# Kernel tuning notes

Hardware: AMD Instinct MI355X
Metric: run time of the kernel (lower is better)

Reference implementation:

```python
import jax, jax.numpy as jnp
import numpy as np

N_VERT, D = 100000, 128
N_EDGE, K, R = 20000, 8, 4


def setup_inputs() -> dict:
    key = jax.random.key(0)
    ks = jax.random.split(key, 16)
    s = 0.05
    return {
        'feats': jax.random.normal(ks[0], (N_VERT, D), dtype=jnp.float32),
        'edge_members': jax.random.randint(ks[1], (N_EDGE, K), 0, N_VERT),
        'adj_members': jax.random.randint(ks[2], (N_EDGE, R, K), 0, N_VERT),
        'ids': jnp.arange(N_EDGE),
        'epoch': 10,
        # VertexConv params (Linear(d,1) each)
        'wq': jax.random.normal(ks[3], (D, 1)) * s, 'bq': jnp.zeros((1,)),
        'wk': jax.random.normal(ks[4], (D, 1)) * s, 'bk': jnp.zeros((1,)),
        'wv': jax.random.normal(ks[5], (D, 1)) * s, 'bv': jnp.zeros((1,)),
        # EdgeConv MLP: Linear(d, d//4) -> ReLU -> Linear(d//4, 1)
        'W1': jax.random.normal(ks[6], (D, D // 4)) * s, 'b1': jnp.zeros((D // 4,)),
        'W2': jax.random.normal(ks[7], (D // 4, 1)) * s, 'b2': jnp.zeros((1,)),
        # final classifier Linear(d, 2)
        'Wfc': jax.random.normal(ks[8], (D, 2)) * s, 'bfc': jnp.zeros((2,)),
    }


def _vertex_conv(feats, members, wq, bq, wk, bk, wv, bv):
    # members: [E, K] vertex indices; aggregates each hyperedge's vertices into one feature.
    f = feats[members]                         # [E,K,d] irregular gather
    q = f @ wq + bq                            # [E,K,1]
    k = f @ wk + bk                            # [E,K,1]
    v = f @ wv + bv                            # [E,K,1]
    # score[e,j,l] = q[e,j]*k[e,l]; original softmaxes over the K-1 "other" vertices (l != j)
    S = q * jnp.swapaxes(k, -1, -2)            # [E,K,K]
    S = jnp.where(jnp.eye(members.shape[-1], dtype=bool), -jnp.inf, S)
    a = jax.nn.softmax(S, axis=-1)             # [E,K,K]
    di = jnp.tanh(jnp.einsum('ejl,elo->ejo', a, v))  # [E,K,1] per-vertex scalar gate
    return (di * f).sum(axis=1)                # [E,d]


def reference(feats, edge_members, adj_members, ids, epoch,
              wq, bq, wk, bk, wv, bv, W1, b1, W2, b2, Wfc, bfc):
    n = edge_members.shape[0]
    # epoch >= wu_e(=0): hyperedge feature from edge_dict
    xn = _vertex_conv(feats, edge_members, wq, bq, wk, bk, wv, bv)   # [N,d]
    # epoch >= wu_a(=5): hyperedge features from each vertex's adjacent edges
    xe = _vertex_conv(feats, adj_members.reshape(n * R, K),
                      wq, bq, wk, bk, wv, bv).reshape(n, R, -1)       # [N,R,d]
    ft = jnp.concatenate([xn[:, None, :], xe], axis=1)                # [N,1+R,d]
    # EdgeConv: attention over the 1+R candidate hyperedge feats
    sc = jax.nn.relu(ft @ W1 + b1) @ W2 + b2                          # [N,1+R,1]
    a = jax.nn.softmax(sc, axis=1)
    h = (a * ft).sum(axis=1)                                          # [N,d]
    # dropout in eval mode (identity), then sigmoid(Linear(d,2))
    return jax.nn.sigmoid(h @ Wfc + bfc)                              # [N,2]
```

## Files before the change

kernel.cpp:

```cpp
#include <hip/hip_runtime.h>
#include <math.h>

#define KK 8
#define DD 128
#define RR 4
#define NG 5
#define HID 32
#define NSLOT 48

typedef __attribute__((ext_vector_type(8))) short short8_t;
typedef __attribute__((ext_vector_type(4))) float f32x4_t;

__device__ __forceinline__ unsigned short f2bf(float x) {
    unsigned int u = __float_as_uint(x);
    unsigned int r = (u + 0x7FFFu + ((u >> 16) & 1u)) >> 16;
    return (unsigned short)r;
}
__device__ __forceinline__ float bf2f(unsigned short u) {
    return __uint_as_float((unsigned int)u << 16);
}
__device__ __forceinline__ float fexp(float x) { return __expf(x); }
__device__ __forceinline__ float frcp(float x) { return __builtin_amdgcn_rcpf(x); }
__device__ __forceinline__ float ftanh(float x) {
    const float xx = fminf(fmaxf(x, -10.f), 10.f);
    const float e2 = __expf(2.f * xx);
    return (e2 - 1.f) * __builtin_amdgcn_rcpf(e2 + 1.f);
}

__global__ __launch_bounds__(256) void proj_mfma(
    const float* __restrict__ feats, int n_vert, int n_tg,
    const float* __restrict__ wq, const float* __restrict__ wk,
    const float* __restrict__ wv, const float* __restrict__ Wfc,
    const float* __restrict__ W1,
    const float* __restrict__ bq, const float* __restrict__ bk,
    const float* __restrict__ bv,
    unsigned short* __restrict__ proj)
{
    __shared__ short Bsh[12 * 64 * 8];

    const int t = threadIdx.x;
    const int wave = t >> 6, lane = t & 63;
    const int row = lane & 15;
    const int kg  = lane >> 4;

    #pragma unroll
    for (int q = 0; q < 3; ++q) {
        const int p = t + q * 256;
        const int ntks = p >> 6, plane = p & 63;
        const int nt = ntks >> 2, ks = ntks & 3;
        const int n  = nt * 16 + (plane & 15);
        const int k0 = ks * 32 + (plane >> 4) * 8;
        short8_t v;
        #pragma unroll
        for (int j = 0; j < 8; ++j) {
            const int k = k0 + j;
            float val;
            if      (n == 0) val = wq[k];
            else if (n == 1) val = wk[k];
            else if (n == 2) val = wv[k];
            else if (n == 3) val = Wfc[2 * k];
            else if (n == 4) val = Wfc[2 * k + 1];
            else if (n < 37) val = W1[k * HID + (n - 5)];
            else             val = 0.f;
            v[j] = (short)f2bf(val);
        }
        *(short8_t*)&Bsh[p * 8] = v;
    }

    const float bq0 = bq[0], bk0 = bk[0], bv0 = bv[0];
    __syncthreads();

    for (int tg = blockIdx.x; tg < n_tg; tg += gridDim.x) {
        const int mbase = (tg * 4 + wave) * 16;
        if (mbase >= n_vert) continue;

        long long arow = (long long)(mbase + row);
        if (arow >= n_vert) arow = n_vert - 1;
        const float* ar = &feats[arow * DD + kg * 8];
        float4 araw[8];
        #pragma unroll
        for (int ks = 0; ks < 4; ++ks) {
            araw[2 * ks]     = *(const float4*)&ar[ks * 32];
            araw[2 * ks + 1] = *(const float4*)&ar[ks * 32 + 4];
        }

        short8_t afrag[4];
        #pragma unroll
        for (int ks = 0; ks < 4; ++ks) {
            const float4 x0 = araw[2 * ks], x1 = araw[2 * ks + 1];
            short8_t a;
            a[0] = (short)f2bf(x0.x); a[1] = (short)f2bf(x0.y);
            a[2] = (short)f2bf(x0.z); a[3] = (short)f2bf(x0.w);
            a[4] = (short)f2bf(x1.x); a[5] = (short)f2bf(x1.y);
            a[6] = (short)f2bf(x1.z); a[7] = (short)f2bf(x1.w);
            afrag[ks] = a;
        }

        #pragma unroll
        for (int nt = 0; nt < 3; ++nt) {
            f32x4_t acc = {0.f, 0.f, 0.f, 0.f};
            #pragma unroll
            for (int ks = 0; ks < 4; ++ks) {
                const short8_t b = *(const short8_t*)&Bsh[((nt * 4 + ks) * 64 + lane) * 8];
                acc = __builtin_amdgcn_mfma_f32_16x16x32_bf16(afrag[ks], b, acc, 0, 0, 0);
            }
            const int col = nt * 16 + row;
            if (col < 37) {
                const int slot = (col < 5) ? col : (col + 3);
                float badd = 0.f;
                if      (col == 0) badd = bq0;
                else if (col == 1) badd = bk0;
                else if (col == 2) badd = bv0;
                #pragma unroll
                for (int r = 0; r < 4; ++r) {
                    const int vr = mbase + kg * 4 + r;
                    if (vr < n_vert)
                        proj[(long long)vr * NSLOT + slot] = f2bf(acc[r] + badd);
                }
            }
        }
    }
}

__global__ __launch_bounds__(256) void edge_fused(
    const int* __restrict__ edge_members,
    const int* __restrict__ adj_members,
    const unsigned short* __restrict__ proj,
    const float* __restrict__ b1, const float* __restrict__ W2,
    const float* __restrict__ b2, const float* __restrict__ bfc,
    float* __restrict__ out, int n_edge)
{
    __shared__ unsigned vidS[4][NG * KK];
    __shared__ float diS [4][NG * KK];
    __shared__ float ftfcS[4][NG][2];
    __shared__ float scS [4][NG];

    const int t = threadIdx.x;
    const int w = t >> 6;
    const int lane = t & 63;
    const int e = blockIdx.x * 4 + w;
    if (e >= n_edge) return;

    const int g = lane >> 3;
    const int j = lane & 7;
    const bool act = lane < NG * KK;

    int vid = 0;
    if (act) vid = (g == 0) ? edge_members[e * KK + j]
                            : adj_members[((e * RR) + (g - 1)) * KK + j];

    const char* projB = (const char*)proj;
    const unsigned vOff = (unsigned)vid * (NSLOT * 2u);

    const uint4 qpu = *(const uint4*)(projB + vOff);

    if (act) vidS[w][lane] = vOff;
    asm volatile("s_waitcnt lgkmcnt(0)" ::: "memory");

    const int m = lane & 31;
    const int h = lane >> 5;
    const unsigned mOff = 16u + 2u * (unsigned)m;
    float pv2[3][KK];
    #pragma unroll
    for (int p = 0; p < 3; ++p) {
        const int grp = (p << 1) | h;
        if (grp < NG) {
            #pragma unroll
            for (int r = 0; r < KK; ++r) {
                const unsigned off = vidS[w][grp * KK + r] + mOff;
                pv2[p][r] = bf2f(*(const unsigned short*)(projB + off));
            }
        }
    }

    const float qv  = bf2f((unsigned short)(qpu.x & 0xFFFFu));
    const float kv  = bf2f((unsigned short)(qpu.x >> 16));
    const float vv  = bf2f((unsigned short)(qpu.y & 0xFFFFu));
    const float pf0 = bf2f((unsigned short)(qpu.y >> 16));
    const float pf1 = bf2f((unsigned short)(qpu.z & 0xFFFFu));

    float k8[KK], v8[KK];
    #pragma unroll
    for (int r = 0; r < KK; ++r) {
        k8[r] = __shfl(kv, (g << 3) + r);
        v8[r] = __shfl(vv, (g << 3) + r);
    }
    float mx = -1e30f;
    float s[KK];
    #pragma unroll
    for (int r = 0; r < KK; ++r) {
        s[r] = qv * k8[r];
        if (r != j) mx = fmaxf(mx, s[r]);
    }
    float den = 0.f, num = 0.f;
    #pragma unroll
    for (int r = 0; r < KK; ++r) {
        if (r == j) continue;
        const float ex = fexp(s[r] - mx);
        den += ex;
        num += ex * v8[r];
    }
    const float di = ftanh(num * frcp(den));

    float px = di * pf0, py = di * pf1;
    #pragma unroll
    for (int mm = 4; mm >= 1; mm >>= 1) {
        px += __shfl_xor(px, mm);
        py += __shfl_xor(py, mm);
    }
    if (act) {
        diS[w][lane] = di;
        if (j == 0) { ftfcS[w][g][0] = px; ftfcS[w][g][1] = py; }
    }
    asm volatile("s_waitcnt lgkmcnt(0)" ::: "memory");

    const float b1m = b1[m];
    const float w2m = W2[m];
    #pragma unroll
    for (int p = 0; p < 3; ++p) {
        const int grp = (p << 1) | h;
        if (grp < NG) {
            float acc = 0.f;
            #pragma unroll
            for (int r = 0; r < KK; ++r)
                acc += diS[w][grp * KK + r] * pv2[p][r];
            float hid = fmaxf(acc + b1m, 0.f) * w2m;
            #pragma unroll
            for (int mm = 16; mm >= 1; mm >>= 1) hid += __shfl_xor(hid, mm);
            if (m == 0) scS[w][grp] = hid + b2[0];
        }
    }
    asm volatile("s_waitcnt lgkmcnt(0)" ::: "memory");

    if (lane < 2) {
        float sc0[NG];
        float m5 = -1e30f;
        #pragma unroll
        for (int gg = 0; gg < NG; ++gg) { sc0[gg] = scS[w][gg]; m5 = fmaxf(m5, sc0[gg]); }
        float ssum = 0.f;
        #pragma unroll
        for (int gg = 0; gg < NG; ++gg) { sc0[gg] = fexp(sc0[gg] - m5); ssum += sc0[gg]; }
        const float inv = frcp(ssum);
        float hc = 0.f;
        #pragma unroll
        for (int gg = 0; gg < NG; ++gg) hc += sc0[gg] * inv * ftfcS[w][gg][lane];
        const float z = hc + bfc[lane];
        out[e * 2 + lane] = frcp(1.f + fexp(-z));
    }
}

extern "C" void kernel_launch(void* const* d_in, const int* in_sizes, int n_in,
                              void* d_out, int out_size, void* d_ws, size_t ws_size,
                              hipStream_t stream) {
    const float* feats        = (const float*)d_in[0];
    const int*   edge_members = (const int*)  d_in[1];
    const int*   adj_members  = (const int*)  d_in[2];
    const float* wq  = (const float*)d_in[5];
    const float* bq  = (const float*)d_in[6];
    const float* wk  = (const float*)d_in[7];
    const float* bk  = (const float*)d_in[8];
    const float* wv  = (const float*)d_in[9];
    const float* bv  = (const float*)d_in[10];
    const float* W1  = (const float*)d_in[11];
    const float* b1  = (const float*)d_in[12];
    const float* W2  = (const float*)d_in[13];
    const float* b2  = (const float*)d_in[14];
    const float* Wfc = (const float*)d_in[15];
    const float* bfc = (const float*)d_in[16];
    float* out = (float*)d_out;

    const int n_vert = in_sizes[0] / DD;
    const int n_edge = in_sizes[1] / KK;

    unsigned short* proj = (unsigned short*)d_ws;

    const int n_mtiles = (n_vert + 15) / 16;
    const int n_tg = (n_mtiles + 3) / 4;
    const int grid = (n_tg < 640) ? n_tg : 640;

    proj_mfma<<<grid, 256, 0, stream>>>(
        feats, n_vert, n_tg, wq, wk, wv, Wfc, W1, bq, bk, bv, proj);

    edge_fused<<<(n_edge + 3) / 4, 256, 0, stream>>>(
        edge_members, adj_members, proj, b1, W2, b2, bfc, out, n_edge);
}
```

Before: 39.82 us.

## Pack eight edges per 320-thread block to remove idle lanes in edge kernel

```diff
diff --git a/kernel.cpp b/kernel.cpp
--- a/kernel.cpp
+++ b/kernel.cpp
@@ -7,6 +7,7 @@
 #define NG 5
 #define HID 32
 #define NSLOT 48
+#define EPB 8
 
 typedef __attribute__((ext_vector_type(8))) short short8_t;
 typedef __attribute__((ext_vector_type(4))) float f32x4_t;
@@ -122,7 +123,7 @@
     }
 }
 
-__global__ __launch_bounds__(256) void edge_fused(
+__global__ __launch_bounds__(320) void edge_fused(
     const int* __restrict__ edge_members,
     const int* __restrict__ adj_members,
     const unsigned short* __restrict__ proj,
@@ -130,46 +131,45 @@
     const float* __restrict__ b2, const float* __restrict__ bfc,
     float* __restrict__ out, int n_edge)
 {
-    __shared__ unsigned vidS[4][NG * KK];
-    __shared__ float diS [4][NG * KK];
-    __shared__ float ftfcS[4][NG][2];
-    __shared__ float scS [4][NG];
+    __shared__ unsigned vidS[EPB * NG][KK];
+    __shared__ float    diS [EPB * NG][KK];
+    __shared__ float    ftfcS[EPB][NG][2];
+    __shared__ float    scS [EPB][NG];
 
     const int t = threadIdx.x;
-    const int w = t >> 6;
     const int lane = t & 63;
-    const int e = blockIdx.x * 4 + w;
-    if (e >= n_edge) return;
-
-    const int g = lane >> 3;
-    const int j = lane & 7;
-    const bool act = lane < NG * KK;
-
-    int vid = 0;
-    if (act) vid = (g == 0) ? edge_members[e * KK + j]
-                            : adj_members[((e * RR) + (g - 1)) * KK + j];
+    const int gs = t >> 3;
+    const int j  = t & 7;
+    const int es = gs / 5;
+    const int g  = gs % 5;
+
+    int e = blockIdx.x * EPB + es;
+    const bool ev = (e < n_edge);
+    if (!ev) e = n_edge - 1;
+
+    const int vid = (g == 0) ? edge_members[e * KK + j]
+                             : adj_members[((e * RR) + (g - 1)) * KK + j];
 
     const char* projB = (const char*)proj;
     const unsigned vOff = (unsigned)vid * (NSLOT * 2u);
 
     const uint4 qpu = *(const uint4*)(projB + vOff);
 
-    if (act) vidS[w][lane] = vOff;
+    vidS[gs][j] = vOff;
     asm volatile("s_waitcnt lgkmcnt(0)" ::: "memory");
 
-    const int m = lane & 31;
-    const int h = lane >> 5;
+    const int m  = lane & 31;
+    const int hh = lane >> 5;
+    const int gmBase = (t >> 6) * 8;
     const unsigned mOff = 16u + 2u * (unsigned)m;
-    float pv2[3][KK];
-    #pragma unroll
-    for (int p = 0; p < 3; ++p) {
-        const int grp = (p << 1) | h;
-        if (grp < NG) {
-            #pragma unroll
-            for (int r = 0; r < KK; ++r) {
-                const unsigned off = vidS[w][grp * KK + r] + mOff;
-                pv2[p][r] = bf2f(*(const unsigned short*)(projB + off));
-            }
+    float pv2[4][KK];
+    #pragma unroll
+    for (int p = 0; p < 4; ++p) {
+        const int gm = gmBase + p * 2 + hh;
+        #pragma unroll
+        for (int r = 0; r < KK; ++r) {
+            const unsigned off = vidS[gm][r] + mOff;
+            pv2[p][r] = bf2f(*(const unsigned short*)(projB + off));
         }
     }
 
@@ -179,11 +179,12 @@
     const float pf0 = bf2f((unsigned short)(qpu.y >> 16));
     const float pf1 = bf2f((unsigned short)(qpu.z & 0xFFFFu));
 
+    const int gb = lane & ~7;
     float k8[KK], v8[KK];
     #pragma unroll
     for (int r = 0; r < KK; ++r) {
-        k8[r] = __shfl(kv, (g << 3) + r);
-        v8[r] = __shfl(vv, (g << 3) + r);
+        k8[r] = __shfl(kv, gb + r);
+        v8[r] = __shfl(vv, gb + r);
     }
     float mx = -1e30f;
     float s[KK];
@@ -208,44 +209,44 @@
         px += __shfl_xor(px, mm);
         py += __shfl_xor(py, mm);
     }
-    if (act) {
-        diS[w][lane] = di;
-        if (j == 0) { ftfcS[w][g][0] = px; ftfcS[w][g][1] = py; }
-    }
+    diS[gs][j] = di;
+    if (j == 0) { ftfcS[es][g][0] = px; ftfcS[es][g][1] = py; }
     asm volatile("s_waitcnt lgkmcnt(0)" ::: "memory");
 
     const float b1m = b1[m];
     const float w2m = W2[m];
     #pragma unroll
-    for (int p = 0; p < 3; ++p) {
-        const int grp = (p << 1) | h;
-        if (grp < NG) {
-            float acc = 0.f;
+    for (int p = 0; p < 4; ++p) {
+        const int gm = gmBase + p * 2 + hh;
+        float acc = 0.f;
+        #pragma unroll
+        for (int r = 0; r < KK; ++r)
+            acc += diS[gm][r] * pv2[p][r];
+        float hid = fmaxf(acc + b1m, 0.f) * w2m;
+        #pragma unroll
+        for (int mm = 16; mm >= 1; mm >>= 1) hid += __shfl_xor(hid, mm);
+        if (m == 0) scS[gm / 5][gm % 5] = hid + b2[0];
+    }
+    __syncthreads();
+
+    if (t < EPB * 2) {
+        const int es2 = t >> 1, c = t & 1;
+        const int e2 = blockIdx.x * EPB + es2;
+        if (e2 < n_edge) {
+            float sc0[NG];
+            float m5 = -1e30f;
             #pragma unroll
-            for (int r = 0; r < KK; ++r)
-                acc += diS[w][grp * KK + r] * pv2[p][r];
-            float hid = fmaxf(acc + b1m, 0.f) * w2m;
+            for (int gg = 0; gg < NG; ++gg) { sc0[gg] = scS[es2][gg]; m5 = fmaxf(m5, sc0[gg]); }
+            float ssum = 0.f, hc = 0.f;
             #pragma unroll
-            for (int mm = 16; mm >= 1; mm >>= 1) hid += __shfl_xor(hid, mm);
-            if (m == 0) scS[w][grp] = hid + b2[0];
-        }
-    }
-    asm volatile("s_waitcnt lgkmcnt(0)" ::: "memory");
-
-    if (lane < 2) {
-        float sc0[NG];
-        float m5 = -1e30f;
-        #pragma unroll
-        for (int gg = 0; gg < NG; ++gg) { sc0[gg] = scS[w][gg]; m5 = fmaxf(m5, sc0[gg]); }
-        float ssum = 0.f;
-        #pragma unroll
-        for (int gg = 0; gg < NG; ++gg) { sc0[gg] = fexp(sc0[gg] - m5); ssum += sc0[gg]; }
-        const float inv = frcp(ssum);
-        float hc = 0.f;
-        #pragma unroll
-        for (int gg = 0; gg < NG; ++gg) hc += sc0[gg] * inv * ftfcS[w][gg][lane];
-        const float z = hc + bfc[lane];
-        out[e * 2 + lane] = frcp(1.f + fexp(-z));
+            for (int gg = 0; gg < NG; ++gg) {
+                const float a = fexp(sc0[gg] - m5);
+                ssum += a;
+                hc += a * ftfcS[es2][gg][c];
+            }
+            const float z = hc * frcp(ssum) + bfc[c];
+            out[e2 * 2 + c] = frcp(1.f + fexp(-z));
+        }
     }
 }
 
@@ -281,6 +282,6 @@
     proj_mfma<<<grid, 256, 0, stream>>>(
         feats, n_vert, n_tg, wq, wk, wv, Wfc, W1, bq, bk, bv, proj);
 
-    edge_fused<<<(n_edge + 3) / 4, 256, 0, stream>>>(
+    edge_fused<<<(n_edge + EPB - 1) / EPB, 320, 0, stream>>>(
         edge_members, adj_members, proj, b1, W2, b2, bfc, out, n_edge);
 }
```

Result: slower. 42.54 us (+6.8%).
